# Performance work log

Measured on AMD Instinct MI355X. Metric: run time of the kernel, lower is better.

Reference implementation:

```python
import jax, jax.numpy as jnp
import numpy as np

N, B, C = 512, 256, 64          # num_nodes, batch, in_dim (= out_dim since out_dim arg is 0)
CK3, CK4 = C // 2, C            # c_k = int(d**(k-L)*in_dim), d=2, S=2, L=4 -> k=3:32, k=4:64
EPS = 1e-5                      # BatchNorm1d eps


def _ring_hop_indices():
    # Ring graph: node i adjacent to i+-1. DFS hop sets (as the torch __find_k_hops computes):
    #   <=S-hop set (S=2, includes self): [i, i-1, i-2, i+1, i+2]
    #   exact-k sets for k=3,4: [i-k, i+k]
    i = np.arange(N)
    idx_S = np.stack([i, (i - 1) % N, (i - 2) % N, (i + 1) % N, (i + 2) % N], axis=1)
    idx_L3 = np.stack([(i - 3) % N, (i + 3) % N], axis=1)
    idx_L4 = np.stack([(i - 4) % N, (i + 4) % N], axis=1)
    return (jnp.asarray(idx_S, jnp.int32), jnp.asarray(idx_L3, jnp.int32), jnp.asarray(idx_L4, jnp.int32))


def setup_inputs() -> dict:
    key = jax.random.key(0)
    ks = jax.random.split(key, 6)
    idx_S, idx_L3, idx_L4 = _ring_hop_indices()
    s = 1.0 / np.sqrt(C)  # xavier-ish scale
    return {
        "features": jax.random.normal(ks[0], (B, N, C), jnp.float32),
        "A": jax.random.uniform(ks[1], (B, N, N), jnp.float32),
        "W_S": jax.random.normal(ks[2], (N, 5, C, C), jnp.float32) * s,
        "W_L3": jax.random.normal(ks[3], (N, 2, C, CK3), jnp.float32) * s,
        "W_L4": jax.random.normal(ks[4], (N, 2, C, CK4), jnp.float32) * s,
        "Wa": jax.random.normal(ks[5], (C + CK3 + CK4, C), jnp.float32) * s,
        "bn_gamma": jnp.ones((C,), jnp.float32),
        "bn_beta": jnp.zeros((C,), jnp.float32),
        "prelu_a": jnp.full((1,), 0.25, jnp.float32),
        "idx_S": idx_S,
        "idx_L3": idx_L3,
        "idx_L4": idx_L4,
    }


def _hop_mix(features, A, idx, W):
    # features: [B,N,C]; idx: [N,M]; W: [N,M,C,Co]
    g = features[:, idx]                                   # [B,N,M,C]  per-node neighbor gather
    a = A[:, jnp.arange(idx.shape[0])[:, None], idx]       # [B,N,M]    adjacency edge weights
    # sum_m a[b,n,m] * (g[b,n,m,:] @ W[n,m,:,:])
    return jnp.einsum('bnm,bnmc,nmcd->bnd', a, g, W)


def reference(features, A, W_S, W_L3, W_L4, Wa, bn_gamma, bn_beta, prelu_a, idx_S, idx_L3, idx_L4):
    H_S = _hop_mix(features, A, idx_S, W_S)                                   # [B,N,C]
    H_L = jnp.concatenate([_hop_mix(features, A, idx_L3, W_L3),
                           _hop_mix(features, A, idx_L4, W_L4)], axis=-1)     # [B,N,CK3+CK4]
    H_a = jnp.concatenate([H_S, H_L], axis=-1)                                # [B,N,C+total_L]
    H = jnp.einsum('bnf,fo->bno', H_a, Wa)                                    # [B,N,C]
    # BatchNorm1d (training mode): stats over (batch, nodes) per channel, biased variance
    mean = H.mean(axis=(0, 1))
    var = H.var(axis=(0, 1))
    Hn = (H - mean) * jax.lax.rsqrt(var + EPS) * bn_gamma + bn_beta
    # PReLU with a single shared learnable slope
    return jnp.where(Hn > 0, Hn, prelu_a * Hn)
```

## Files before the change

kernel.cpp:

```cpp
#include <hip/hip_runtime.h>
#include <hip/hip_bf16.h>

#define NN 512
#define BB 256

typedef unsigned short u16;
typedef unsigned int u32;
typedef __attribute__((ext_vector_type(8))) short bf16x8;
typedef __attribute__((ext_vector_type(4))) short u16x4;
typedef __attribute__((ext_vector_type(4))) float f32x4;
typedef __attribute__((ext_vector_type(4))) u32 u32x4;

__device__ __forceinline__ u16 f2bf(float x){
  u32 u = __builtin_bit_cast(u32, x);
  u32 r = u + 0x7fffu + ((u >> 16) & 1u);
  return (u16)(r >> 16);
}
__device__ __forceinline__ float bf2f(u16 h){
  return __builtin_bit_cast(float, (u32)h << 16);
}
__device__ __forceinline__ u32 cvtpk(float lo, float hi){
  float2 t; t.x = lo; t.y = hi;
  __hip_bfloat162 h = __float22bfloat162_rn(t);
  u32 r;
  __builtin_memcpy(&r, &h, 4);
  return r;
}
__device__ __forceinline__ bf16x8 pack8nc(float4 u, float4 v){
  u32x4 w;
  w[0] = cvtpk(u.x, u.y);
  w[1] = cvtpk(u.z, u.w);
  w[2] = cvtpk(v.x, v.y);
  w[3] = cvtpk(v.z, v.w);
  return __builtin_bit_cast(bf16x8, w);
}

__global__ __launch_bounds__(256) void k_cast(const float* __restrict__ f, u16* __restrict__ fb){
  int i = blockIdx.x * 256 + threadIdx.x;
  const float4* p = (const float4*)f;
  float4 a = p[2*i], b = p[2*i+1];
  uint4 o;
  o.x = cvtpk(a.x, a.y); o.y = cvtpk(a.z, a.w);
  o.z = cvtpk(b.x, b.y); o.w = cvtpk(b.z, b.w);
  ((uint4*)fb)[i] = o;
}

__global__ __launch_bounds__(256) void k_wat(const float* __restrict__ Wa, u16* __restrict__ wat){
  int t = blockIdx.x * 256 + threadIdx.x;
  int o = t / 192, r = t - o * 192;
  int blk = r >> 6, q = r & 63;
  float v = 0.f;
  if (blk == 0) v = Wa[q * 64 + o];
  else if (blk == 1) { if (q < 32) v = Wa[(64 + q) * 64 + o]; }
  else v = Wa[(96 + q) * 64 + o];
  wat[t] = f2bf(v);
}

__global__ __launch_bounds__(512, 4) void k_main(
    const u16* __restrict__ fb, const float* __restrict__ A,
    const float* __restrict__ WS, const float* __restrict__ WL3, const float* __restrict__ WL4,
    const u16* __restrict__ wat,
    const int* __restrict__ idxS, const int* __restrict__ idxL3, const int* __restrict__ idxL4,
    u16* __restrict__ H, float* __restrict__ bn_part)
{
  int bid = blockIdx.x;
  int n = (bid & 7) * 64 + (bid >> 3);
  int tid = threadIdx.x, lane = tid & 63, wv = tid >> 6;
  int l15 = lane & 15, lg = lane >> 4;

  __shared__ u16 wl[9 * 4096];
  __shared__ u16 albf[9 * 256 + 64];
  __shared__ int nbrl[12];

  if (tid < 9){
    int v;
    if (tid < 5) v = idxS[n * 5 + tid];
    else if (tid < 7) v = idxL3[n * 2 + (tid - 5)];
    else v = idxL4[n * 2 + (tid - 7)];
    nbrl[tid] = v;
  }

  if (tid < 256){
    int b = tid;
    const float* Ab = A + (size_t)b * (NN * NN) + (size_t)n * NN;
    #pragma unroll
    for (int j = 0; j < 9; ++j){
      int nb;
      if (j < 5) nb = idxS[n * 5 + j];
      else if (j < 7) nb = idxL3[n * 2 + (j - 5)];
      else nb = idxL4[n * 2 + (j - 7)];
      albf[j * 256 + b] = f2bf(Ab[nb]);
    }
  }

  for (int jj = wv; jj < 9; jj += (wv == 7 ? 1 : 16)){
    const float* src; int jb, cstride;
    if (jj < 5)      { src = WS  + ((size_t)n * 5 + jj)       * 4096; jb = 0; cstride = 64; }
    else if (jj < 7) { src = WL3 + ((size_t)n * 2 + (jj - 5)) * 2048; jb = 1; cstride = 32; }
    else             { src = WL4 + ((size_t)n * 2 + (jj - 7)) * 4096; jb = 2; cstride = 64; }
    char* wlj = (char*)wl + jj * 8192;

    bf16x8 bw[4][2];
    #pragma unroll
    for (int ni = 0; ni < 4; ++ni){
      int c = ni * 16 + l15;
      const float* p = src + c * cstride + lg * 8;
      float4 u = *(const float4*)p, v = *(const float4*)(p + 4);
      bw[ni][0] = pack8nc(u, v);
      if (jb != 1){
        float4 u1 = *(const float4*)(p + 32), v1 = *(const float4*)(p + 36);
        bw[ni][1] = pack8nc(u1, v1);
      }
    }
    #pragma unroll
    for (int h = 0; h < 2; ++h){
      f32x4 fa[2][4];
      #pragma unroll
      for (int mi = 0; mi < 2; ++mi)
        #pragma unroll
        for (int ni = 0; ni < 4; ++ni){ fa[mi][ni][0]=0.f; fa[mi][ni][1]=0.f; fa[mi][ni][2]=0.f; fa[mi][ni][3]=0.f; }
      #pragma unroll
      for (int ks = 0; ks < 2; ++ks){
        if (jb == 1 && ks == 1) continue;
        bf16x8 af0 = *(const bf16x8*)(wat + (h * 32 + l15) * 192      + jb * 64 + ks * 32 + lg * 8);
        bf16x8 af1 = *(const bf16x8*)(wat + (h * 32 + 16 + l15) * 192 + jb * 64 + ks * 32 + lg * 8);
        #pragma unroll
        for (int ni = 0; ni < 4; ++ni){
          fa[0][ni] = __builtin_amdgcn_mfma_f32_16x16x32_bf16(af0, bw[ni][ks], fa[0][ni], 0, 0, 0);
          fa[1][ni] = __builtin_amdgcn_mfma_f32_16x16x32_bf16(af1, bw[ni][ks], fa[1][ni], 0, 0, 0);
        }
      }
      #pragma unroll
      for (int mi = 0; mi < 2; ++mi)
        #pragma unroll
        for (int ni = 0; ni < 4; ++ni)
          #pragma unroll
          for (int r = 0; r < 4; ++r){
            int o = h * 32 + mi * 16 + lg * 4 + r;
            int c = ni * 16 + l15;
            *(u16*)(wlj + o * 128 + ((2 * c) ^ ((o & 7) << 4))) = f2bf(fa[mi][ni][r]);
          }
    }
  }
  __syncthreads();

  int rb = wv * 32;
  const size_t XROW = (size_t)NN * 64;
  const u16* xb0 = fb + (size_t)(rb + l15) * XROW + lg * 8;
  const u16* xb1 = xb0 + (size_t)16 * XROW;

  f32x4 acc[2][4];
  #pragma unroll
  for (int mi = 0; mi < 2; ++mi)
    #pragma unroll
    for (int ni = 0; ni < 4; ++ni){ acc[mi][ni][0]=0.f; acc[mi][ni][1]=0.f; acc[mi][ni][2]=0.f; acc[mi][ni][3]=0.f; }
  f32x4 kz; kz[0]=0.f; kz[1]=0.f; kz[2]=0.f; kz[3]=0.f;

  #pragma unroll 1
  for (int j = 0; j < 9; ++j){
    int nbrj = nbrl[j];
    const char* wlj = (const char*)wl + j * 8192;

    f32x4 avc[2];
    #pragma unroll
    for (int mi = 0; mi < 2; ++mi){
      u16x4 a4 = *(const u16x4*)(albf + j * 256 + rb + mi * 16 + lg * 4);
      avc[mi][0] = bf2f((u16)a4[0]); avc[mi][1] = bf2f((u16)a4[1]);
      avc[mi][2] = bf2f((u16)a4[2]); avc[mi][3] = bf2f((u16)a4[3]);
    }
    bf16x8 ax[2][2];
    ax[0][0] = *(const bf16x8*)(xb0 + nbrj * 64);
    ax[0][1] = *(const bf16x8*)(xb0 + nbrj * 64 + 32);
    ax[1][0] = *(const bf16x8*)(xb1 + nbrj * 64);
    ax[1][1] = *(const bf16x8*)(xb1 + nbrj * 64 + 32);
    bf16x8 bfr[2][4];
    #pragma unroll
    for (int ks = 0; ks < 2; ++ks)
      #pragma unroll
      for (int ni = 0; ni < 4; ++ni){
        int d = ni * 16 + l15;
        bfr[ks][ni] = *(const bf16x8*)(wlj + d * 128 + ((ks * 64 + lg * 16) ^ ((d & 7) << 4)));
      }

    #pragma unroll
    for (int mi = 0; mi < 2; ++mi){
      f32x4 P[4];
      #pragma unroll
      for (int ni = 0; ni < 4; ++ni){
        P[ni] = __builtin_amdgcn_mfma_f32_16x16x32_bf16(ax[mi][0], bfr[0][ni], kz, 0, 0, 0);
        P[ni] = __builtin_amdgcn_mfma_f32_16x16x32_bf16(ax[mi][1], bfr[1][ni], P[ni], 0, 0, 0);
      }
      #pragma unroll
      for (int ni = 0; ni < 4; ++ni){
        acc[mi][ni][0] += avc[mi][0] * P[ni][0];
        acc[mi][ni][1] += avc[mi][1] * P[ni][1];
        acc[mi][ni][2] += avc[mi][2] * P[ni][2];
        acc[mi][ni][3] += avc[mi][3] * P[ni][3];
      }
    }
  }

  #pragma unroll
  for (int mi = 0; mi < 2; ++mi)
    #pragma unroll
    for (int r = 0; r < 4; ++r){
      int bl = rb + mi * 16 + lg * 4 + r;
      u16* Hr = H + (size_t)bl * (NN * 64) + n * 64;
      #pragma unroll
      for (int ni = 0; ni < 4; ++ni)
        Hr[ni * 16 + l15] = f2bf(acc[mi][ni][r]);
    }

  __syncthreads();
  float* bnl = (float*)albf;
  #pragma unroll
  for (int ni = 0; ni < 4; ++ni){
    float s = 0.f, sq = 0.f;
    #pragma unroll
    for (int mi = 0; mi < 2; ++mi)
      #pragma unroll
      for (int r = 0; r < 4; ++r){ float v = acc[mi][ni][r]; s += v; sq += v * v; }
    s  += __shfl_xor(s, 16);  s  += __shfl_xor(s, 32);
    sq += __shfl_xor(sq, 16); sq += __shfl_xor(sq, 32);
    if (lane < 16){
      bnl[wv * 128 + ni * 16 + lane]      = s;
      bnl[wv * 128 + 64 + ni * 16 + lane] = sq;
    }
  }
  __syncthreads();
  if (tid < 128){
    float s = 0.f;
    #pragma unroll
    for (int w = 0; w < 8; ++w) s += bnl[w * 128 + tid];
    bn_part[(size_t)bid * 128 + tid] = s;
  }
}

__global__ __launch_bounds__(1024) void k_reduce(const float* __restrict__ bn, const float* __restrict__ gamma,
    const float* __restrict__ beta, float* __restrict__ ss){
  __shared__ float red[2048];
  int t = threadIdx.x, d = t & 63, part = t >> 6;
  float s = 0.f, sq = 0.f;
  for (int w = part; w < 512; w += 16){
    s  += bn[w * 128 + d];
    sq += bn[w * 128 + 64 + d];
  }
  red[t] = s; red[1024 + t] = sq;
  __syncthreads();
  if (t < 64){
    float S = 0.f, SQ = 0.f;
    #pragma unroll
    for (int p = 0; p < 16; ++p){ S += red[p * 64 + t]; SQ += red[1024 + p * 64 + t]; }
    float mean = S * (1.f / 131072.f);
    float var  = SQ * (1.f / 131072.f) - mean * mean;
    float sc = gamma[t] * rsqrtf(var + 1e-5f);
    ss[t] = sc;
    ss[64 + t] = beta[t] - mean * sc;
  }
}

__global__ __launch_bounds__(256) void k_apply(const u16* __restrict__ H, const float* __restrict__ ss,
    const float* __restrict__ pa, float* __restrict__ out){
  float a = pa[0];
  int i = blockIdx.x * 256 + threadIdx.x;
  uint4 v = ((const uint4*)H)[i];
  int d0 = (i << 3) & 63;
  float4 sc0 = *(const float4*)(ss + d0);
  float4 sc1 = *(const float4*)(ss + d0 + 4);
  float4 sh0 = *(const float4*)(ss + 64 + d0);
  float4 sh1 = *(const float4*)(ss + 68 + d0);
  float4 o0, o1; float y;
  y = bf2f((u16)(v.x & 0xffff)) * sc0.x + sh0.x; o0.x = y > 0.f ? y : a * y;
  y = bf2f((u16)(v.x >> 16))    * sc0.y + sh0.y; o0.y = y > 0.f ? y : a * y;
  y = bf2f((u16)(v.y & 0xffff)) * sc0.z + sh0.z; o0.z = y > 0.f ? y : a * y;
  y = bf2f((u16)(v.y >> 16))    * sc0.w + sh0.w; o0.w = y > 0.f ? y : a * y;
  y = bf2f((u16)(v.z & 0xffff)) * sc1.x + sh1.x; o1.x = y > 0.f ? y : a * y;
  y = bf2f((u16)(v.z >> 16))    * sc1.y + sh1.y; o1.y = y > 0.f ? y : a * y;
  y = bf2f((u16)(v.w & 0xffff)) * sc1.z + sh1.z; o1.z = y > 0.f ? y : a * y;
  y = bf2f((u16)(v.w >> 16))    * sc1.w + sh1.w; o1.w = y > 0.f ? y : a * y;
  ((float4*)out)[2 * i]     = o0;
  ((float4*)out)[2 * i + 1] = o1;
}

extern "C" void kernel_launch(void* const* d_in, const int* in_sizes, int n_in,
                              void* d_out, int out_size, void* d_ws, size_t ws_size,
                              hipStream_t stream){
  const float* f     = (const float*)d_in[0];
  const float* A     = (const float*)d_in[1];
  const float* WS    = (const float*)d_in[2];
  const float* WL3   = (const float*)d_in[3];
  const float* WL4   = (const float*)d_in[4];
  const float* Wa    = (const float*)d_in[5];
  const float* gamma = (const float*)d_in[6];
  const float* beta  = (const float*)d_in[7];
  const float* pa    = (const float*)d_in[8];
  const int* idxS    = (const int*)d_in[9];
  const int* idxL3   = (const int*)d_in[10];
  const int* idxL4   = (const int*)d_in[11];

  char* ws = (char*)d_ws;
  u16*   fbb = (u16*)(ws);
  u16*   Hb  = (u16*)(ws + 16777216);
  u16*   wat = (u16*)(ws + 33554432);
  float* bnp = (float*)(ws + 33579008);
  float* sss = (float*)(ws + 33841152);

  k_cast  <<<4096, 256, 0, stream>>>(f, fbb);
  k_wat   <<<48,   256, 0, stream>>>(Wa, wat);
  k_main  <<<512,  512, 0, stream>>>(fbb, A, WS, WL3, WL4, wat, idxS, idxL3, idxL4, Hb, bnp);
  k_reduce<<<1,   1024, 0, stream>>>(bnp, gamma, beta, sss);
  k_apply <<<4096, 256, 0, stream>>>(Hb, sss, pa, (float*)d_out);
}
```

Baseline: 76.38 us.

## Fuse main, BN reduction and apply via cooperative grid sync; halve weight LDS

Merges the cast and Wa-transpose kernels into one prep launch. The main kernel becomes a cooperative launch that computes partial BN stats, grid-syncs, reduces the per-channel statistics across 64 blocks, grid-syncs again, and applies normalization and PReLU directly from the register accumulators. This avoids writing and re-reading the bf16 H intermediate and saves two launches. The folded-weight LDS buffer is cut from 9 to 5 slices by folding the weights in two phases, which is meant to raise occupancy so all 512 blocks can be co-resident for the grid sync. If the cooperative launch fails, it falls back to the old split path.

```diff
diff --git a/kernel.cpp b/kernel.cpp
--- a/kernel.cpp
+++ b/kernel.cpp
@@ -1,5 +1,8 @@
 #include <hip/hip_runtime.h>
 #include <hip/hip_bf16.h>
+#include <hip/hip_cooperative_groups.h>
+
+namespace cg = cooperative_groups;
 
 #define NN 512
 #define BB 256
@@ -35,40 +38,97 @@
   return __builtin_bit_cast(bf16x8, w);
 }
 
-__global__ __launch_bounds__(256) void k_cast(const float* __restrict__ f, u16* __restrict__ fb){
-  int i = blockIdx.x * 256 + threadIdx.x;
-  const float4* p = (const float4*)f;
-  float4 a = p[2*i], b = p[2*i+1];
-  uint4 o;
-  o.x = cvtpk(a.x, a.y); o.y = cvtpk(a.z, a.w);
-  o.z = cvtpk(b.x, b.y); o.w = cvtpk(b.z, b.w);
-  ((uint4*)fb)[i] = o;
-}
-
-__global__ __launch_bounds__(256) void k_wat(const float* __restrict__ Wa, u16* __restrict__ wat){
-  int t = blockIdx.x * 256 + threadIdx.x;
-  int o = t / 192, r = t - o * 192;
-  int blk = r >> 6, q = r & 63;
-  float v = 0.f;
-  if (blk == 0) v = Wa[q * 64 + o];
-  else if (blk == 1) { if (q < 32) v = Wa[(64 + q) * 64 + o]; }
-  else v = Wa[(96 + q) * 64 + o];
-  wat[t] = f2bf(v);
-}
-
-__global__ __launch_bounds__(512, 4) void k_main(
+__global__ __launch_bounds__(256) void k_prep(const float* __restrict__ f, u16* __restrict__ fb,
+                                              const float* __restrict__ Wa, u16* __restrict__ wat){
+  int b = blockIdx.x;
+  if (b < 4096){
+    int i = b * 256 + threadIdx.x;
+    const float4* p = (const float4*)f;
+    float4 a = p[2*i], c = p[2*i+1];
+    uint4 o;
+    o.x = cvtpk(a.x, a.y); o.y = cvtpk(a.z, a.w);
+    o.z = cvtpk(c.x, c.y); o.w = cvtpk(c.z, c.w);
+    ((uint4*)fb)[i] = o;
+  } else {
+    int t = (b - 4096) * 256 + threadIdx.x;
+    int o = t / 192, r = t - o * 192;
+    int blk = r >> 6, q = r & 63;
+    float v = 0.f;
+    if (blk == 0) v = Wa[q * 64 + o];
+    else if (blk == 1) { if (q < 32) v = Wa[(64 + q) * 64 + o]; }
+    else v = Wa[(96 + q) * 64 + o];
+    wat[t] = f2bf(v);
+  }
+}
+
+__device__ __forceinline__ void fold_one(int n, int jj, char* wlj, const u16* __restrict__ wat,
+    const float* __restrict__ WS, const float* __restrict__ WL3, const float* __restrict__ WL4,
+    int l15, int lg)
+{
+  const float* src; int jb, cstride;
+  if (jj < 5)      { src = WS  + ((size_t)n * 5 + jj)       * 4096; jb = 0; cstride = 64; }
+  else if (jj < 7) { src = WL3 + ((size_t)n * 2 + (jj - 5)) * 2048; jb = 1; cstride = 32; }
+  else             { src = WL4 + ((size_t)n * 2 + (jj - 7)) * 4096; jb = 2; cstride = 64; }
+
+  bf16x8 bw[4][2];
+  #pragma unroll
+  for (int ni = 0; ni < 4; ++ni){
+    int c = ni * 16 + l15;
+    const float* p = src + c * cstride + lg * 8;
+    float4 u = *(const float4*)p, v = *(const float4*)(p + 4);
+    bw[ni][0] = pack8nc(u, v);
+    if (jb != 1){
+      float4 u1 = *(const float4*)(p + 32), v1 = *(const float4*)(p + 36);
+      bw[ni][1] = pack8nc(u1, v1);
+    }
+  }
+  #pragma unroll
+  for (int h = 0; h < 2; ++h){
+    f32x4 fa[2][4];
+    #pragma unroll
+    for (int mi = 0; mi < 2; ++mi)
+      #pragma unroll
+      for (int ni = 0; ni < 4; ++ni){ fa[mi][ni][0]=0.f; fa[mi][ni][1]=0.f; fa[mi][ni][2]=0.f; fa[mi][ni][3]=0.f; }
+    #pragma unroll
+    for (int ks = 0; ks < 2; ++ks){
+      if (jb == 1 && ks == 1) continue;
+      bf16x8 af0 = *(const bf16x8*)(wat + (h * 32 + l15) * 192      + jb * 64 + ks * 32 + lg * 8);
+      bf16x8 af1 = *(const bf16x8*)(wat + (h * 32 + 16 + l15) * 192 + jb * 64 + ks * 32 + lg * 8);
+      #pragma unroll
+      for (int ni = 0; ni < 4; ++ni){
+        fa[0][ni] = __builtin_amdgcn_mfma_f32_16x16x32_bf16(af0, bw[ni][ks], fa[0][ni], 0, 0, 0);
+        fa[1][ni] = __builtin_amdgcn_mfma_f32_16x16x32_bf16(af1, bw[ni][ks], fa[1][ni], 0, 0, 0);
+      }
+    }
+    #pragma unroll
+    for (int mi = 0; mi < 2; ++mi)
+      #pragma unroll
+      for (int ni = 0; ni < 4; ++ni)
+        #pragma unroll
+        for (int r = 0; r < 4; ++r){
+          int o = h * 32 + mi * 16 + lg * 4 + r;
+          int c = ni * 16 + l15;
+          *(u16*)(wlj + o * 128 + ((2 * c) ^ ((o & 7) << 4))) = f2bf(fa[mi][ni][r]);
+        }
+  }
+}
+
+template<int COOP>
+__device__ __forceinline__ void fused_body(
     const u16* __restrict__ fb, const float* __restrict__ A,
     const float* __restrict__ WS, const float* __restrict__ WL3, const float* __restrict__ WL4,
     const u16* __restrict__ wat,
     const int* __restrict__ idxS, const int* __restrict__ idxL3, const int* __restrict__ idxL4,
-    u16* __restrict__ H, float* __restrict__ bn_part)
+    u16* __restrict__ H, float* __restrict__ bn_part, float* __restrict__ ss,
+    const float* __restrict__ gamma, const float* __restrict__ beta, const float* __restrict__ pa,
+    float* __restrict__ out)
 {
   int bid = blockIdx.x;
   int n = (bid & 7) * 64 + (bid >> 3);
   int tid = threadIdx.x, lane = tid & 63, wv = tid >> 6;
   int l15 = lane & 15, lg = lane >> 4;
 
-  __shared__ u16 wl[9 * 4096];
+  __shared__ u16 wl[5 * 4096];
   __shared__ u16 albf[9 * 256 + 64];
   __shared__ int nbrl[12];
 
@@ -93,55 +153,7 @@
     }
   }
 
-  for (int jj = wv; jj < 9; jj += (wv == 7 ? 1 : 16)){
-    const float* src; int jb, cstride;
-    if (jj < 5)      { src = WS  + ((size_t)n * 5 + jj)       * 4096; jb = 0; cstride = 64; }
-    else if (jj < 7) { src = WL3 + ((size_t)n * 2 + (jj - 5)) * 2048; jb = 1; cstride = 32; }
-    else             { src = WL4 + ((size_t)n * 2 + (jj - 7)) * 4096; jb = 2; cstride = 64; }
-    char* wlj = (char*)wl + jj * 8192;
-
-    bf16x8 bw[4][2];
-    #pragma unroll
-    for (int ni = 0; ni < 4; ++ni){
-      int c = ni * 16 + l15;
-      const float* p = src + c * cstride + lg * 8;
-      float4 u = *(const float4*)p, v = *(const float4*)(p + 4);
-      bw[ni][0] = pack8nc(u, v);
-      if (jb != 1){
-        float4 u1 = *(const float4*)(p + 32), v1 = *(const float4*)(p + 36);
-        bw[ni][1] = pack8nc(u1, v1);
-      }
-    }
-    #pragma unroll
-    for (int h = 0; h < 2; ++h){
-      f32x4 fa[2][4];
-      #pragma unroll
-      for (int mi = 0; mi < 2; ++mi)
-        #pragma unroll
-        for (int ni = 0; ni < 4; ++ni){ fa[mi][ni][0]=0.f; fa[mi][ni][1]=0.f; fa[mi][ni][2]=0.f; fa[mi][ni][3]=0.f; }
-      #pragma unroll
-      for (int ks = 0; ks < 2; ++ks){
-        if (jb == 1 && ks == 1) continue;
-        bf16x8 af0 = *(const bf16x8*)(wat + (h * 32 + l15) * 192      + jb * 64 + ks * 32 + lg * 8);
-        bf16x8 af1 = *(const bf16x8*)(wat + (h * 32 + 16 + l15) * 192 + jb * 64 + ks * 32 + lg * 8);
-        #pragma unroll
-        for (int ni = 0; ni < 4; ++ni){
-          fa[0][ni] = __builtin_amdgcn_mfma_f32_16x16x32_bf16(af0, bw[ni][ks], fa[0][ni], 0, 0, 0);
-          fa[1][ni] = __builtin_amdgcn_mfma_f32_16x16x32_bf16(af1, bw[ni][ks], fa[1][ni], 0, 0, 0);
-        }
-      }
-      #pragma unroll
-      for (int mi = 0; mi < 2; ++mi)
-        #pragma unroll
-        for (int ni = 0; ni < 4; ++ni)
-          #pragma unroll
-          for (int r = 0; r < 4; ++r){
-            int o = h * 32 + mi * 16 + lg * 4 + r;
-            int c = ni * 16 + l15;
-            *(u16*)(wlj + o * 128 + ((2 * c) ^ ((o & 7) << 4))) = f2bf(fa[mi][ni][r]);
-          }
-    }
-  }
+  if (wv < 5) fold_one(n, wv, (char*)wl + wv * 8192, wat, WS, WL3, WL4, l15, lg);
   __syncthreads();
 
   int rb = wv * 32;
@@ -157,59 +169,70 @@
   f32x4 kz; kz[0]=0.f; kz[1]=0.f; kz[2]=0.f; kz[3]=0.f;
 
   #pragma unroll 1
-  for (int j = 0; j < 9; ++j){
-    int nbrj = nbrl[j];
-    const char* wlj = (const char*)wl + j * 8192;
-
-    f32x4 avc[2];
-    #pragma unroll
-    for (int mi = 0; mi < 2; ++mi){
-      u16x4 a4 = *(const u16x4*)(albf + j * 256 + rb + mi * 16 + lg * 4);
-      avc[mi][0] = bf2f((u16)a4[0]); avc[mi][1] = bf2f((u16)a4[1]);
-      avc[mi][2] = bf2f((u16)a4[2]); avc[mi][3] = bf2f((u16)a4[3]);
-    }
-    bf16x8 ax[2][2];
-    ax[0][0] = *(const bf16x8*)(xb0 + nbrj * 64);
-    ax[0][1] = *(const bf16x8*)(xb0 + nbrj * 64 + 32);
-    ax[1][0] = *(const bf16x8*)(xb1 + nbrj * 64);
-    ax[1][1] = *(const bf16x8*)(xb1 + nbrj * 64 + 32);
-    bf16x8 bfr[2][4];
-    #pragma unroll
-    for (int ks = 0; ks < 2; ++ks)
-      #pragma unroll
-      for (int ni = 0; ni < 4; ++ni){
-        int d = ni * 16 + l15;
-        bfr[ks][ni] = *(const bf16x8*)(wlj + d * 128 + ((ks * 64 + lg * 16) ^ ((d & 7) << 4)));
-      }
-
-    #pragma unroll
-    for (int mi = 0; mi < 2; ++mi){
-      f32x4 P[4];
-      #pragma unroll
-      for (int ni = 0; ni < 4; ++ni){
-        P[ni] = __builtin_amdgcn_mfma_f32_16x16x32_bf16(ax[mi][0], bfr[0][ni], kz, 0, 0, 0);
-        P[ni] = __builtin_amdgcn_mfma_f32_16x16x32_bf16(ax[mi][1], bfr[1][ni], P[ni], 0, 0, 0);
-      }
-      #pragma unroll
-      for (int ni = 0; ni < 4; ++ni){
-        acc[mi][ni][0] += avc[mi][0] * P[ni][0];
-        acc[mi][ni][1] += avc[mi][1] * P[ni][1];
-        acc[mi][ni][2] += avc[mi][2] * P[ni][2];
-        acc[mi][ni][3] += avc[mi][3] * P[ni][3];
-      }
-    }
-  }
-
-  #pragma unroll
-  for (int mi = 0; mi < 2; ++mi)
-    #pragma unroll
-    for (int r = 0; r < 4; ++r){
-      int bl = rb + mi * 16 + lg * 4 + r;
-      u16* Hr = H + (size_t)bl * (NN * 64) + n * 64;
-      #pragma unroll
-      for (int ni = 0; ni < 4; ++ni)
-        Hr[ni * 16 + l15] = f2bf(acc[mi][ni][r]);
-    }
+  for (int half = 0; half < 2; ++half){
+    int j0 = half * 5, j1 = half * 5 + (half ? 4 : 5);
+    #pragma unroll 1
+    for (int j = j0; j < j1; ++j){
+      int nbrj = nbrl[j];
+      const char* wlj = (const char*)wl + (j - j0) * 8192;
+
+      f32x4 avc[2];
+      #pragma unroll
+      for (int mi = 0; mi < 2; ++mi){
+        u16x4 a4 = *(const u16x4*)(albf + j * 256 + rb + mi * 16 + lg * 4);
+        avc[mi][0] = bf2f((u16)a4[0]); avc[mi][1] = bf2f((u16)a4[1]);
+        avc[mi][2] = bf2f((u16)a4[2]); avc[mi][3] = bf2f((u16)a4[3]);
+      }
+      bf16x8 ax[2][2];
+      ax[0][0] = *(const bf16x8*)(xb0 + nbrj * 64);
+      ax[0][1] = *(const bf16x8*)(xb0 + nbrj * 64 + 32);
+      ax[1][0] = *(const bf16x8*)(xb1 + nbrj * 64);
+      ax[1][1] = *(const bf16x8*)(xb1 + nbrj * 64 + 32);
+      bf16x8 bfr[2][4];
+      #pragma unroll
+      for (int ks = 0; ks < 2; ++ks)
+        #pragma unroll
+        for (int ni = 0; ni < 4; ++ni){
+          int d = ni * 16 + l15;
+          bfr[ks][ni] = *(const bf16x8*)(wlj + d * 128 + ((ks * 64 + lg * 16) ^ ((d & 7) << 4)));
+        }
+
+      #pragma unroll
+      for (int mi = 0; mi < 2; ++mi){
+        f32x4 P[4];
+        #pragma unroll
+        for (int ni = 0; ni < 4; ++ni){
+          P[ni] = __builtin_amdgcn_mfma_f32_16x16x32_bf16(ax[mi][0], bfr[0][ni], kz, 0, 0, 0);
+          P[ni] = __builtin_amdgcn_mfma_f32_16x16x32_bf16(ax[mi][1], bfr[1][ni], P[ni], 0, 0, 0);
+        }
+        #pragma unroll
+        for (int ni = 0; ni < 4; ++ni){
+          acc[mi][ni][0] += avc[mi][0] * P[ni][0];
+          acc[mi][ni][1] += avc[mi][1] * P[ni][1];
+          acc[mi][ni][2] += avc[mi][2] * P[ni][2];
+          acc[mi][ni][3] += avc[mi][3] * P[ni][3];
+        }
+      }
+    }
+    if (half == 0){
+      __syncthreads();
+      if (wv < 4) fold_one(n, 5 + wv, (char*)wl + wv * 8192, wat, WS, WL3, WL4, l15, lg);
+      __syncthreads();
+    }
+  }
+
+  if (!COOP){
+    #pragma unroll
+    for (int mi = 0; mi < 2; ++mi)
+      #pragma unroll
+      for (int r = 0; r < 4; ++r){
+        int bl = rb + mi * 16 + lg * 4 + r;
+        u16* Hr = H + (size_t)bl * (NN * 64) + n * 64;
+        #pragma unroll
+        for (int ni = 0; ni < 4; ++ni)
+          Hr[ni * 16 + l15] = f2bf(acc[mi][ni][r]);
+      }
+  }
 
   __syncthreads();
   float* bnl = (float*)albf;
@@ -234,6 +257,74 @@
     for (int w = 0; w < 8; ++w) s += bnl[w * 128 + tid];
     bn_part[(size_t)bid * 128 + tid] = s;
   }
+  __threadfence();
+
+  if (COOP){
+    cg::this_grid().sync();
+
+    if (bid < 64){
+      int d = bid;
+      float s  = bn_part[(size_t)tid * 128 + d];
+      float sq = bn_part[(size_t)tid * 128 + 64 + d];
+      #pragma unroll
+      for (int k = 1; k < 64; k <<= 1){
+        s  += __shfl_xor(s, k);
+        sq += __shfl_xor(sq, k);
+      }
+      float* red = (float*)wl;
+      if (lane == 0){ red[wv] = s; red[8 + wv] = sq; }
+      __syncthreads();
+      if (tid == 0){
+        float S = 0.f, SQ = 0.f;
+        #pragma unroll
+        for (int w = 0; w < 8; ++w){ S += red[w]; SQ += red[8 + w]; }
+        float mean = S * (1.f / 131072.f);
+        float var  = SQ * (1.f / 131072.f) - mean * mean;
+        float sc = gamma[d] * rsqrtf(var + 1e-5f);
+        ss[d] = sc;
+        ss[64 + d] = beta[d] - mean * sc;
+        __threadfence();
+      }
+    }
+
+    cg::this_grid().sync();
+
+    float aprelu = pa[0];
+    float scv[4], shv[4];
+    #pragma unroll
+    for (int ni = 0; ni < 4; ++ni){
+      int d = ni * 16 + l15;
+      scv[ni] = ss[d];
+      shv[ni] = ss[64 + d];
+    }
+    #pragma unroll
+    for (int mi = 0; mi < 2; ++mi)
+      #pragma unroll
+      for (int r = 0; r < 4; ++r){
+        int bl = rb + mi * 16 + lg * 4 + r;
+        float* Or = out + (size_t)bl * (NN * 64) + n * 64;
+        #pragma unroll
+        for (int ni = 0; ni < 4; ++ni){
+          float y = acc[mi][ni][r] * scv[ni] + shv[ni];
+          Or[ni * 16 + l15] = y > 0.f ? y : aprelu * y;
+        }
+      }
+  }
+}
+
+__global__ __launch_bounds__(512, 4) void k_fused_coop(
+    const u16* fb, const float* A, const float* WS, const float* WL3, const float* WL4,
+    const u16* wat, const int* idxS, const int* idxL3, const int* idxL4,
+    u16* H, float* bn_part, float* ss, const float* gamma, const float* beta,
+    const float* pa, float* out){
+  fused_body<1>(fb, A, WS, WL3, WL4, wat, idxS, idxL3, idxL4, H, bn_part, ss, gamma, beta, pa, out);
+}
+__global__ __launch_bounds__(512, 4) void k_fused_split(
+    const u16* fb, const float* A, const float* WS, const float* WL3, const float* WL4,
+    const u16* wat, const int* idxS, const int* idxL3, const int* idxL4,
+    u16* H, float* bn_part, float* ss, const float* gamma, const float* beta,
+    const float* pa, float* out){
+  fused_body<0>(fb, A, WS, WL3, WL4, wat, idxS, idxL3, idxL4, H, bn_part, ss, gamma, beta, pa, out);
 }
 
 __global__ __launch_bounds__(1024) void k_reduce(const float* __restrict__ bn, const float* __restrict__ gamma,
@@ -304,10 +395,20 @@
   u16*   wat = (u16*)(ws + 33554432);
   float* bnp = (float*)(ws + 33579008);
   float* sss = (float*)(ws + 33841152);
-
-  k_cast  <<<4096, 256, 0, stream>>>(f, fbb);
-  k_wat   <<<48,   256, 0, stream>>>(Wa, wat);
-  k_main  <<<512,  512, 0, stream>>>(fbb, A, WS, WL3, WL4, wat, idxS, idxL3, idxL4, Hb, bnp);
-  k_reduce<<<1,   1024, 0, stream>>>(bnp, gamma, beta, sss);
-  k_apply <<<4096, 256, 0, stream>>>(Hb, sss, pa, (float*)d_out);
-}
+  float* outp = (float*)d_out;
+
+  k_prep<<<4144, 256, 0, stream>>>(f, fbb, Wa, wat);
+
+  void* args[] = { (void*)&fbb, (void*)&A, (void*)&WS, (void*)&WL3, (void*)&WL4,
+                   (void*)&wat, (void*)&idxS, (void*)&idxL3, (void*)&idxL4,
+                   (void*)&Hb, (void*)&bnp, (void*)&sss, (void*)&gamma, (void*)&beta,
+                   (void*)&pa, (void*)&outp };
+  hipError_t e = hipLaunchCooperativeKernel((const void*)k_fused_coop, dim3(512), dim3(512),
+                                            args, 0, stream);
+  if (e != hipSuccess){
+    k_fused_split<<<512, 512, 0, stream>>>(fbb, A, WS, WL3, WL4, wat, idxS, idxL3, idxL4,
+                                           Hb, bnp, sss, gamma, beta, pa, outp);
+    k_reduce<<<1,   1024, 0, stream>>>(bnp, gamma, beta, sss);
+    k_apply <<<4096, 256, 0, stream>>>(Hb, sss, pa, outp);
+  }
+}
```

After: 263.7 us. +245.2%, slower.

## Halve folded-weight LDS by two-phase fold, split A gather across waves, merge prep kernels

Applied to the files above, without the earlier changes.

Merges the feature cast and Wa transpose kernels into one launch. In k_main the folded weight buffer in LDS shrinks from 9 to 5 slots. The first five hops are folded by waves 0-4 while waves 5-7 gather the adjacency weights in parallel. After processing those hops, waves 4-7 fold the remaining four hops into the reused slots behind two extra barriers. This lowers LDS use per block, which could allow more resident blocks, at the cost of an extra serialized fold phase and more synchronization.

```diff
diff --git a/kernel.cpp b/kernel.cpp
--- a/kernel.cpp
+++ b/kernel.cpp
@@ -35,25 +35,79 @@
   return __builtin_bit_cast(bf16x8, w);
 }
 
-__global__ __launch_bounds__(256) void k_cast(const float* __restrict__ f, u16* __restrict__ fb){
-  int i = blockIdx.x * 256 + threadIdx.x;
-  const float4* p = (const float4*)f;
-  float4 a = p[2*i], b = p[2*i+1];
-  uint4 o;
-  o.x = cvtpk(a.x, a.y); o.y = cvtpk(a.z, a.w);
-  o.z = cvtpk(b.x, b.y); o.w = cvtpk(b.z, b.w);
-  ((uint4*)fb)[i] = o;
-}
-
-__global__ __launch_bounds__(256) void k_wat(const float* __restrict__ Wa, u16* __restrict__ wat){
-  int t = blockIdx.x * 256 + threadIdx.x;
-  int o = t / 192, r = t - o * 192;
-  int blk = r >> 6, q = r & 63;
-  float v = 0.f;
-  if (blk == 0) v = Wa[q * 64 + o];
-  else if (blk == 1) { if (q < 32) v = Wa[(64 + q) * 64 + o]; }
-  else v = Wa[(96 + q) * 64 + o];
-  wat[t] = f2bf(v);
+__global__ __launch_bounds__(256) void k_prep(const float* __restrict__ f, u16* __restrict__ fb,
+                                              const float* __restrict__ Wa, u16* __restrict__ wat){
+  int b = blockIdx.x;
+  if (b < 4096){
+    int i = b * 256 + threadIdx.x;
+    const float4* p = (const float4*)f;
+    float4 a = p[2*i], c = p[2*i+1];
+    uint4 o;
+    o.x = cvtpk(a.x, a.y); o.y = cvtpk(a.z, a.w);
+    o.z = cvtpk(c.x, c.y); o.w = cvtpk(c.z, c.w);
+    ((uint4*)fb)[i] = o;
+  } else {
+    int t = (b - 4096) * 256 + threadIdx.x;
+    int o = t / 192, r = t - o * 192;
+    int blk = r >> 6, q = r & 63;
+    float v = 0.f;
+    if (blk == 0) v = Wa[q * 64 + o];
+    else if (blk == 1) { if (q < 32) v = Wa[(64 + q) * 64 + o]; }
+    else v = Wa[(96 + q) * 64 + o];
+    wat[t] = f2bf(v);
+  }
+}
+
+__device__ __forceinline__ void fold_one(int n, int jj, char* wlj, const u16* __restrict__ wat,
+    const float* __restrict__ WS, const float* __restrict__ WL3, const float* __restrict__ WL4,
+    int l15, int lg)
+{
+  const float* src; int jb, cstride;
+  if (jj < 5)      { src = WS  + ((size_t)n * 5 + jj)       * 4096; jb = 0; cstride = 64; }
+  else if (jj < 7) { src = WL3 + ((size_t)n * 2 + (jj - 5)) * 2048; jb = 1; cstride = 32; }
+  else             { src = WL4 + ((size_t)n * 2 + (jj - 7)) * 4096; jb = 2; cstride = 64; }
+
+  bf16x8 bw[4][2];
+  #pragma unroll
+  for (int ni = 0; ni < 4; ++ni){
+    int c = ni * 16 + l15;
+    const float* p = src + c * cstride + lg * 8;
+    float4 u = *(const float4*)p, v = *(const float4*)(p + 4);
+    bw[ni][0] = pack8nc(u, v);
+    if (jb != 1){
+      float4 u1 = *(const float4*)(p + 32), v1 = *(const float4*)(p + 36);
+      bw[ni][1] = pack8nc(u1, v1);
+    }
+  }
+  #pragma unroll
+  for (int h = 0; h < 2; ++h){
+    f32x4 fa[2][4];
+    #pragma unroll
+    for (int mi = 0; mi < 2; ++mi)
+      #pragma unroll
+      for (int ni = 0; ni < 4; ++ni){ fa[mi][ni][0]=0.f; fa[mi][ni][1]=0.f; fa[mi][ni][2]=0.f; fa[mi][ni][3]=0.f; }
+    #pragma unroll
+    for (int ks = 0; ks < 2; ++ks){
+      if (jb == 1 && ks == 1) continue;
+      bf16x8 af0 = *(const bf16x8*)(wat + (h * 32 + l15) * 192      + jb * 64 + ks * 32 + lg * 8);
+      bf16x8 af1 = *(const bf16x8*)(wat + (h * 32 + 16 + l15) * 192 + jb * 64 + ks * 32 + lg * 8);
+      #pragma unroll
+      for (int ni = 0; ni < 4; ++ni){
+        fa[0][ni] = __builtin_amdgcn_mfma_f32_16x16x32_bf16(af0, bw[ni][ks], fa[0][ni], 0, 0, 0);
+        fa[1][ni] = __builtin_amdgcn_mfma_f32_16x16x32_bf16(af1, bw[ni][ks], fa[1][ni], 0, 0, 0);
+      }
+    }
+    #pragma unroll
+    for (int mi = 0; mi < 2; ++mi)
+      #pragma unroll
+      for (int ni = 0; ni < 4; ++ni)
+        #pragma unroll
+        for (int r = 0; r < 4; ++r){
+          int o = h * 32 + mi * 16 + lg * 4 + r;
+          int c = ni * 16 + l15;
+          *(u16*)(wlj + o * 128 + ((2 * c) ^ ((o & 7) << 4))) = f2bf(fa[mi][ni][r]);
+        }
+  }
 }
 
 __global__ __launch_bounds__(512, 4) void k_main(
@@ -68,7 +122,7 @@
   int tid = threadIdx.x, lane = tid & 63, wv = tid >> 6;
   int l15 = lane & 15, lg = lane >> 4;
 
-  __shared__ u16 wl[9 * 4096];
+  __shared__ u16 wl[5 * 4096];
   __shared__ u16 albf[9 * 256 + 64];
   __shared__ int nbrl[12];
 
@@ -80,68 +134,25 @@
     nbrl[tid] = v;
   }
 
-  if (tid < 256){
-    int b = tid;
-    const float* Ab = A + (size_t)b * (NN * NN) + (size_t)n * NN;
-    #pragma unroll
-    for (int j = 0; j < 9; ++j){
-      int nb;
-      if (j < 5) nb = idxS[n * 5 + j];
-      else if (j < 7) nb = idxL3[n * 2 + (j - 5)];
-      else nb = idxL4[n * 2 + (j - 7)];
-      albf[j * 256 + b] = f2bf(Ab[nb]);
-    }
-  }
-
-  for (int jj = wv; jj < 9; jj += (wv == 7 ? 1 : 16)){
-    const float* src; int jb, cstride;
-    if (jj < 5)      { src = WS  + ((size_t)n * 5 + jj)       * 4096; jb = 0; cstride = 64; }
-    else if (jj < 7) { src = WL3 + ((size_t)n * 2 + (jj - 5)) * 2048; jb = 1; cstride = 32; }
-    else             { src = WL4 + ((size_t)n * 2 + (jj - 7)) * 4096; jb = 2; cstride = 64; }
-    char* wlj = (char*)wl + jj * 8192;
-
-    bf16x8 bw[4][2];
-    #pragma unroll
-    for (int ni = 0; ni < 4; ++ni){
-      int c = ni * 16 + l15;
-      const float* p = src + c * cstride + lg * 8;
-      float4 u = *(const float4*)p, v = *(const float4*)(p + 4);
-      bw[ni][0] = pack8nc(u, v);
-      if (jb != 1){
-        float4 u1 = *(const float4*)(p + 32), v1 = *(const float4*)(p + 36);
-        bw[ni][1] = pack8nc(u1, v1);
+  if (wv >= 5){
+    int i = tid - 320;
+    #pragma unroll
+    for (int rep = 0; rep < 2; ++rep){
+      int b = (rep == 0) ? i : i + 192;
+      if (rep == 1 && i >= 64) break;
+      const float* Ab = A + (size_t)b * (NN * NN) + (size_t)n * NN;
+      #pragma unroll
+      for (int j = 0; j < 9; ++j){
+        int nb;
+        if (j < 5) nb = idxS[n * 5 + j];
+        else if (j < 7) nb = idxL3[n * 2 + (j - 5)];
+        else nb = idxL4[n * 2 + (j - 7)];
+        albf[j * 256 + b] = f2bf(Ab[nb]);
       }
     }
-    #pragma unroll
-    for (int h = 0; h < 2; ++h){
-      f32x4 fa[2][4];
-      #pragma unroll
-      for (int mi = 0; mi < 2; ++mi)
-        #pragma unroll
-        for (int ni = 0; ni < 4; ++ni){ fa[mi][ni][0]=0.f; fa[mi][ni][1]=0.f; fa[mi][ni][2]=0.f; fa[mi][ni][3]=0.f; }
-      #pragma unroll
-      for (int ks = 0; ks < 2; ++ks){
-        if (jb == 1 && ks == 1) continue;
-        bf16x8 af0 = *(const bf16x8*)(wat + (h * 32 + l15) * 192      + jb * 64 + ks * 32 + lg * 8);
-        bf16x8 af1 = *(const bf16x8*)(wat + (h * 32 + 16 + l15) * 192 + jb * 64 + ks * 32 + lg * 8);
-        #pragma unroll
-        for (int ni = 0; ni < 4; ++ni){
-          fa[0][ni] = __builtin_amdgcn_mfma_f32_16x16x32_bf16(af0, bw[ni][ks], fa[0][ni], 0, 0, 0);
-          fa[1][ni] = __builtin_amdgcn_mfma_f32_16x16x32_bf16(af1, bw[ni][ks], fa[1][ni], 0, 0, 0);
-        }
-      }
-      #pragma unroll
-      for (int mi = 0; mi < 2; ++mi)
-        #pragma unroll
-        for (int ni = 0; ni < 4; ++ni)
-          #pragma unroll
-          for (int r = 0; r < 4; ++r){
-            int o = h * 32 + mi * 16 + lg * 4 + r;
-            int c = ni * 16 + l15;
-            *(u16*)(wlj + o * 128 + ((2 * c) ^ ((o & 7) << 4))) = f2bf(fa[mi][ni][r]);
-          }
-    }
-  }
+  }
+
+  if (wv < 5) fold_one(n, wv, (char*)wl + wv * 8192, wat, WS, WL3, WL4, l15, lg);
   __syncthreads();
 
   int rb = wv * 32;
@@ -157,46 +168,55 @@
   f32x4 kz; kz[0]=0.f; kz[1]=0.f; kz[2]=0.f; kz[3]=0.f;
 
   #pragma unroll 1
-  for (int j = 0; j < 9; ++j){
-    int nbrj = nbrl[j];
-    const char* wlj = (const char*)wl + j * 8192;
-
-    f32x4 avc[2];
-    #pragma unroll
-    for (int mi = 0; mi < 2; ++mi){
-      u16x4 a4 = *(const u16x4*)(albf + j * 256 + rb + mi * 16 + lg * 4);
-      avc[mi][0] = bf2f((u16)a4[0]); avc[mi][1] = bf2f((u16)a4[1]);
-      avc[mi][2] = bf2f((u16)a4[2]); avc[mi][3] = bf2f((u16)a4[3]);
-    }
-    bf16x8 ax[2][2];
-    ax[0][0] = *(const bf16x8*)(xb0 + nbrj * 64);
-    ax[0][1] = *(const bf16x8*)(xb0 + nbrj * 64 + 32);
-    ax[1][0] = *(const bf16x8*)(xb1 + nbrj * 64);
-    ax[1][1] = *(const bf16x8*)(xb1 + nbrj * 64 + 32);
-    bf16x8 bfr[2][4];
-    #pragma unroll
-    for (int ks = 0; ks < 2; ++ks)
-      #pragma unroll
-      for (int ni = 0; ni < 4; ++ni){
-        int d = ni * 16 + l15;
-        bfr[ks][ni] = *(const bf16x8*)(wlj + d * 128 + ((ks * 64 + lg * 16) ^ ((d & 7) << 4)));
+  for (int half = 0; half < 2; ++half){
+    int j0 = half * 5, j1 = half * 5 + (half ? 4 : 5);
+    #pragma unroll 1
+    for (int j = j0; j < j1; ++j){
+      int nbrj = nbrl[j];
+      const char* wlj = (const char*)wl + (j - j0) * 8192;
+
+      f32x4 avc[2];
+      #pragma unroll
+      for (int mi = 0; mi < 2; ++mi){
+        u16x4 a4 = *(const u16x4*)(albf + j * 256 + rb + mi * 16 + lg * 4);
+        avc[mi][0] = bf2f((u16)a4[0]); avc[mi][1] = bf2f((u16)a4[1]);
+        avc[mi][2] = bf2f((u16)a4[2]); avc[mi][3] = bf2f((u16)a4[3]);
       }
-
-    #pragma unroll
-    for (int mi = 0; mi < 2; ++mi){
-      f32x4 P[4];
-      #pragma unroll
-      for (int ni = 0; ni < 4; ++ni){
-        P[ni] = __builtin_amdgcn_mfma_f32_16x16x32_bf16(ax[mi][0], bfr[0][ni], kz, 0, 0, 0);
-        P[ni] = __builtin_amdgcn_mfma_f32_16x16x32_bf16(ax[mi][1], bfr[1][ni], P[ni], 0, 0, 0);
+      bf16x8 ax[2][2];
+      ax[0][0] = *(const bf16x8*)(xb0 + nbrj * 64);
+      ax[0][1] = *(const bf16x8*)(xb0 + nbrj * 64 + 32);
+      ax[1][0] = *(const bf16x8*)(xb1 + nbrj * 64);
+      ax[1][1] = *(const bf16x8*)(xb1 + nbrj * 64 + 32);
+      bf16x8 bfr[2][4];
+      #pragma unroll
+      for (int ks = 0; ks < 2; ++ks)
+        #pragma unroll
+        for (int ni = 0; ni < 4; ++ni){
+          int d = ni * 16 + l15;
+          bfr[ks][ni] = *(const bf16x8*)(wlj + d * 128 + ((ks * 64 + lg * 16) ^ ((d & 7) << 4)));
+        }
+
+      #pragma unroll
+      for (int mi = 0; mi < 2; ++mi){
+        f32x4 P[4];
+        #pragma unroll
+        for (int ni = 0; ni < 4; ++ni){
+          P[ni] = __builtin_amdgcn_mfma_f32_16x16x32_bf16(ax[mi][0], bfr[0][ni], kz, 0, 0, 0);
+          P[ni] = __builtin_amdgcn_mfma_f32_16x16x32_bf16(ax[mi][1], bfr[1][ni], P[ni], 0, 0, 0);
+        }
+        #pragma unroll
+        for (int ni = 0; ni < 4; ++ni){
+          acc[mi][ni][0] += avc[mi][0] * P[ni][0];
+          acc[mi][ni][1] += avc[mi][1] * P[ni][1];
+          acc[mi][ni][2] += avc[mi][2] * P[ni][2];
+          acc[mi][ni][3] += avc[mi][3] * P[ni][3];
+        }
       }
-      #pragma unroll
-      for (int ni = 0; ni < 4; ++ni){
-        acc[mi][ni][0] += avc[mi][0] * P[ni][0];
-        acc[mi][ni][1] += avc[mi][1] * P[ni][1];
-        acc[mi][ni][2] += avc[mi][2] * P[ni][2];
-        acc[mi][ni][3] += avc[mi][3] * P[ni][3];
-      }
+    }
+    if (half == 0){
+      __syncthreads();
+      if (wv >= 4) fold_one(n, wv + 1, (char*)wl + (wv - 4) * 8192, wat, WS, WL3, WL4, l15, lg);
+      __syncthreads();
     }
   }
 
@@ -305,8 +325,7 @@
   float* bnp = (float*)(ws + 33579008);
   float* sss = (float*)(ws + 33841152);
 
-  k_cast  <<<4096, 256, 0, stream>>>(f, fbb);
-  k_wat   <<<48,   256, 0, stream>>>(Wa, wat);
+  k_prep  <<<4144, 256, 0, stream>>>(f, fbb, Wa, wat);
   k_main  <<<512,  512, 0, stream>>>(fbb, A, WS, WL3, WL4, wat, idxS, idxL3, idxL4, Hb, bnp);
   k_reduce<<<1,   1024, 0, stream>>>(bnp, gamma, beta, sss);
   k_apply <<<4096, 256, 0, stream>>>(Hb, sss, pa, (float*)d_out);
```

After: 91.75 us. 1.2x slower.
